# Optimization experiments

Measured on AMD Instinct MI355X. Metric: run time of the kernel, lower is better.

The kernel has to match this reference:

```python
import jax, jax.numpy as jnp
import numpy as np

SCALES = (1, 2, 4, 8, 16)
BETA = 0.25
RESI = 0.5  # Phi(embed_dim, 0.5) -> resi_ratio = 0.5


def _cubic(x):
    # PyTorch bicubic kernel, A = -0.75
    A = -0.75
    x = jnp.abs(x)
    return jnp.where(
        x <= 1.0,
        ((A + 2.0) * x - (A + 3.0)) * x * x + 1.0,
        jnp.where(x < 2.0, A * (((x - 5.0) * x + 8.0) * x - 4.0), 0.0),
    )


def _resize_axis_bicubic(x, axis, out_size):
    # Separable bicubic upsample matching F.interpolate(mode='bicubic', align_corners=False)
    in_size = x.shape[axis]
    scale = in_size / out_size
    src = (jnp.arange(out_size, dtype=jnp.float32) + 0.5) * scale - 0.5
    i0 = jnp.floor(src).astype(jnp.int32)
    frac = src - i0.astype(jnp.float32)
    offs = jnp.arange(-1, 3)
    idx = jnp.clip(i0[:, None] + offs[None, :], 0, in_size - 1)   # [out, 4]
    w = _cubic(frac[:, None] - offs[None, :].astype(jnp.float32))  # [out, 4], rows sum to 1
    g = jnp.take(x, idx, axis=axis)  # axis dim replaced by (out, 4)
    wshape = [1] * g.ndim
    wshape[axis] = out_size
    wshape[axis + 1] = 4
    return jnp.sum(g * w.reshape(wshape), axis=axis + 1)


def _bicubic(x, H, W):
    return _resize_axis_bicubic(_resize_axis_bicubic(x, 2, H), 3, W)


def _phi(x, w, b):
    # Phi: h*(1-r) + conv3x3(h)*r
    y = jax.lax.conv_general_dilated(
        x, w, (1, 1), 'SAME', dimension_numbers=('NCHW', 'OIHW', 'NCHW'))
    return x * (1.0 - RESI) + (y + b[None, :, None, None]) * RESI


def _mse(a, b):
    return jnp.mean((a - b) ** 2)


def _forward(z, emb_weight, phi_w, phi_b):
    B, C, H, W = z.shape
    K = len(SCALES)
    # PhiPartiallyShared ticks for 4 shared convs (K != 4 branch uses 1/3/K spacing)
    ticks = np.linspace(1.0 / (3.0 * 4), 1.0 - 1.0 / (3.0 * 4), 4)
    sg = jax.lax.stop_gradient
    z_d = sg(z)
    z_res = z_d
    z_hat = jnp.zeros_like(z_d)
    emb_sq = jnp.sum(emb_weight * emb_weight, axis=1)  # [n_e]
    loss = jnp.zeros((), z.dtype)
    idx_list = []
    for si, ph in enumerate(SCALES):
        if si != K - 1:
            f = H // ph  # 'area' interpolate == exact average pooling (ph divides H)
            r = z_res.reshape(B, C, ph, f, ph, f).mean(axis=(3, 5))
        else:
            r = z_res
        rf = r.transpose(0, 2, 3, 1).reshape(-1, C)  # [B*ph*ph, C]
        # argmin of cdist == argmin of ||e||^2 - 2 r.e (||r||^2 constant per row)
        d = emb_sq[None, :] - 2.0 * (rf @ emb_weight.T)  # [N, n_e]
        idx = jnp.argmin(d, axis=1)
        q = emb_weight[idx].reshape(B, ph, ph, C).transpose(0, 3, 1, 2)  # [B,C,ph,ph]
        if si != K - 1:
            q = _bicubic(q, H, W)
        pi = int(np.argmin(np.abs(ticks - si / (K - 1))))  # static Phi selection
        q = _phi(q, phi_w[pi], phi_b[pi])
        z_hat = z_hat + q
        z_res = z_res - sg(q)
        idx_list.append(idx.reshape(B, -1))
        loss = loss + BETA * _mse(sg(z_hat), z) + _mse(z_hat, z_d)
    loss = loss / K
    z_hat_st = sg(z_hat - z_d) + z  # straight-through
    return z_hat_st, loss, jnp.concatenate(idx_list, axis=1)


def setup_inputs():
    key = jax.random.key(0)
    k1, k2, k3, k4 = jax.random.split(key, 4)
    z = jax.random.normal(k1, (64, 32, 16, 16), jnp.float32)
    emb_weight = jax.random.normal(k2, (4096, 32), jnp.float32)
    phi_w = jax.random.normal(k3, (4, 32, 32, 3, 3), jnp.float32) * 0.05
    phi_b = jax.random.normal(k4, (4, 32), jnp.float32) * 0.01
    return {"z": z, "emb_weight": emb_weight, "phi_w": phi_w, "phi_b": phi_b}


def reference(z, emb_weight, phi_w, phi_b):
    return _forward(z, emb_weight, phi_w, phi_b)
```

## Files before the change

kernel.cpp:

```cpp
#include <hip/hip_runtime.h>

#define NB 64
#define NC 32
#define NH 16
#define NW 16
#define NE 4096
#define NTOT (NB*NC*NH*NW)
#define IDXW 341
#define GRID 256
#define TPB 1024

typedef float f32x2 __attribute__((ext_vector_type(2)));
typedef float f32x4 __attribute__((ext_vector_type(4)));

__device__ __forceinline__ f32x2 pkfma(f32x2 a, f32x2 b, f32x2 c) {
#if __has_builtin(__builtin_elementwise_fma)
  return __builtin_elementwise_fma(a, b, c);
#else
  return (f32x2){fmaf(a.x, b.x, c.x), fmaf(a.y, b.y, c.y)};
#endif
}

__device__ __forceinline__ double cubicw(double x) {
  const double A = -0.75;
  x = fabs(x);
  if (x <= 1.0) return ((A + 2.0) * x - (A + 3.0)) * x * x + 1.0;
  if (x < 2.0)  return A * (((x - 5.0) * x + 8.0) * x - 4.0);
  return 0.0;
}

__device__ __forceinline__ unsigned monokey(float f) {
  unsigned u = __float_as_uint(f);
  return (u & 0x80000000u) ? ~u : (u | 0x80000000u);
}

__device__ __forceinline__ unsigned aload(unsigned* p) {
  return __hip_atomic_load(p, __ATOMIC_RELAXED, __HIP_MEMORY_SCOPE_AGENT);
}

__device__ __forceinline__ void groupbar(unsigned* fl) {
  __syncthreads();
  if (threadIdx.x == 0) {
    __hip_atomic_fetch_add(fl, 1u, __ATOMIC_RELAXED, __HIP_MEMORY_SCOPE_AGENT);
    while (aload(fl) < 4u) __builtin_amdgcn_s_sleep(1);
  }
  __syncthreads();
}

__global__ __launch_bounds__(TPB)
__attribute__((amdgpu_waves_per_eu(4, 4)))
void k_fused(
    const float* __restrict__ z, const float* __restrict__ emb,
    const float* __restrict__ phi_w, const float* __restrict__ phi_b,
    double* __restrict__ rv64, double* __restrict__ emb_sq,
    double* __restrict__ loss_d, float* __restrict__ emb_ti,
    float* __restrict__ emb_sq32, int* __restrict__ win,
    unsigned* __restrict__ cnt, unsigned* __restrict__ gbar,
    unsigned* __restrict__ flags,
    float* __restrict__ out_zhat, float* __restrict__ out_loss,
    float* __restrict__ out_idx)
{
  __shared__ double lds[8192];
  double* zres = lds;
  char* qreg   = (char*)lds + 16384;
  char* ttreg  = (char*)lds + 49152;

  const int tid = threadIdx.x;
  const int b = blockIdx.x & 63, jq = blockIdx.x >> 6;
  const int co0 = jq * 8;

  if (tid < 16) atomicCAS(&flags[(b << 4) + tid], 0xAAAAAAAAu, 0u);
  if (tid == 0) {
    atomicCAS((unsigned long long*)loss_d, 0xAAAAAAAAAAAAAAAAull, 0ull);
    atomicCAS(cnt, 0xAAAAAAAAu, 0u);
    atomicCAS(gbar, 0xAAAAAAAAu, 0u);
  }

  #pragma unroll
  for (int t = 0; t < 2; t++) {
    int i = t * TPB + tid;
    zres[i] = (double)z[((b * NC + co0) << 8) + i];
  }
  {
    int c0 = blockIdx.x * 16;
    if (tid < 512) {
      int cl = tid >> 5, k = tid & 31;
      emb_ti[(k >> 1) * 8192 + (c0 + cl) * 2 + (k & 1)] = emb[(c0 + cl) * NC + k];
    }
    if (tid < 16) {
      const float* er = emb + (c0 + tid) * NC;
      double s = 0.0;
      #pragma unroll
      for (int j = 0; j < 8; j++)
        s += (double)er[4*j]*er[4*j] + (double)er[4*j+1]*er[4*j+1]
           + (double)er[4*j+2]*er[4*j+2] + (double)er[4*j+3]*er[4*j+3];
      emb_sq[c0 + tid] = s;
      emb_sq32[c0 + tid] = (float)s;
    }
  }
  __syncthreads();
  if (tid == 0) {
    __threadfence();
    __hip_atomic_fetch_add(&flags[(b << 4) + 15], 1u, __ATOMIC_RELAXED,
                           __HIP_MEMORY_SCOPE_AGENT);
    if (jq == 0) {
      while (aload(&flags[(b << 4) + 15]) < 4u) __builtin_amdgcn_s_sleep(1);
      __hip_atomic_fetch_add(gbar, 1u, __ATOMIC_RELAXED,
                             __HIP_MEMORY_SCOPE_AGENT);
      while (aload(gbar) < 64u) __builtin_amdgcn_s_sleep(4);
      __hip_atomic_store(&flags[(b << 4) + 14], 1u, __ATOMIC_RELAXED,
                         __HIP_MEMORY_SCOPE_AGENT);
    } else {
      while (aload(&flags[(b << 4) + 14]) < 1u) __builtin_amdgcn_s_sleep(1);
    }
    __threadfence();
  }
  __syncthreads();

  double bloss = 0.0;
  const int pis[5]  = {0, 1, 2, 2, 3};
  const int offs[5] = {0, 1, 5, 21, 85};

  for (int si = 0; si < 5; si++) {
    const int ph = 1 << si, f = NH / ph, ph2 = ph * ph;
    const int idx_off = offs[si];

    if (si == 4) {
      #pragma unroll
      for (int t = 0; t < 2; t++) {
        int i = t * TPB + tid;
        int pix = i >> 3, cc = i & 7;
        __hip_atomic_store(&rv64[(((b << 8) + pix) << 5) + co0 + cc],
                           zres[cc * 256 + pix],
                           __ATOMIC_RELAXED, __HIP_MEMORY_SCOPE_AGENT);
      }
    } else {
      double* pp = (double*)qreg;
      double* pooled = (double*)(qreg + 8192);
      const int P = (f >= 8) ? 8 : f;
      const int lP = (f >= 8) ? 3 : ((f == 4) ? 2 : 1);
      const int items = 8 * ph2, work = items * P, dpp = f / P;
      if (tid < work) {
        int it = tid >> lP, part = tid & (P - 1);
        int cc = it >> (2 * si), rem = it & (ph2 - 1);
        int y = rem >> si, x = rem & (ph - 1);
        const double* basep = zres + cc * 256 + (y * f) * 16 + x * f;
        double s = 0.0;
        for (int dy = part * dpp; dy < part * dpp + dpp; dy++) {
          const double* rp = basep + dy * 16;
          #pragma unroll 4
          for (int dx = 0; dx < f; dx++) s += rp[dx];
        }
        pp[tid] = s;
      }
      __syncthreads();
      if (tid < items) {
        double s = 0.0;
        for (int p2 = 0; p2 < P; p2++) s += pp[(tid << lP) + p2];
        pooled[tid] = s / (double)(f * f);
      }
      __syncthreads();
      if (tid < items) {
        int rem = tid >> 3, cc = tid & 7;
        __hip_atomic_store(&rv64[(((b << 8) + rem) << 5) + co0 + cc],
                           pooled[cc * ph2 + rem],
                           __ATOMIC_RELAXED, __HIP_MEMORY_SCOPE_AGENT);
      }
    }
    groupbar(&flags[(b << 4) + si * 2]);

    {
      const int count = (ph2 > jq) ? ((ph2 - jq + 3) >> 2) : 0;
      float*  rvt32 = (float*)qreg;
      double* rvt64 = (double*)(qreg + 8192);
      unsigned long long* wdu = (unsigned long long*)(qreg + 24576);
      unsigned short* cand = (unsigned short*)(qreg + 26624);
      for (int t = tid; t < 2048; t += TPB) {
        int m = t >> 5, k = t & 31;
        double v = __hip_atomic_load(&rv64[(((b << 8) + jq + 4 * m) << 5) + k],
                                     __ATOMIC_RELAXED, __HIP_MEMORY_SCOPE_AGENT);
        rvt64[t] = v;
        rvt32[t] = (float)v;
      }
      __syncthreads();
      if (count) {
        const int e0 = tid << 2;
        const f32x4 es4 = *(const f32x4*)(emb_sq32 + e0);
        const int lane = tid & 63, wv_ = tid >> 6;
        for (int m0 = 0; m0 < count; m0 += 8) {
          #pragma unroll
          for (int jg = 0; jg < 2; jg++) {
            f32x4 acc[4];
            #pragma unroll
            for (int j = 0; j < 4; j++) acc[j] = (f32x4){0.f, 0.f, 0.f, 0.f};
            const f32x4* __restrict__ eb = (const f32x4*)emb_ti + (tid << 1);
            #pragma unroll 4
            for (int k2 = 0; k2 < 16; k2++) {
              f32x4 E0 = eb[k2 * 2048];
              f32x4 E1 = eb[k2 * 2048 + 1];
              #pragma unroll
              for (int j = 0; j < 4; j++) {
                f32x2 r2 = *(const f32x2*)(rvt32 + ((m0 + jg * 4 + j) << 5)
                                           + (k2 << 1));
                f32x2 lo = {acc[j].x, acc[j].y}, hi = {acc[j].z, acc[j].w};
                lo = pkfma((f32x2){r2.x, r2.x}, (f32x2){E0.x, E0.z}, lo);
                lo = pkfma((f32x2){r2.y, r2.y}, (f32x2){E0.y, E0.w}, lo);
                hi = pkfma((f32x2){r2.x, r2.x}, (f32x2){E1.x, E1.z}, hi);
                hi = pkfma((f32x2){r2.y, r2.y}, (f32x2){E1.y, E1.w}, hi);
                acc[j] = (f32x4){lo.x, lo.y, hi.x, hi.y};
              }
            }
            #pragma unroll
            for (int j = 0; j < 4; j++) {
              float d0 = es4.x - 2.f * acc[j].x;
              float d1 = es4.y - 2.f * acc[j].y;
              float d2 = es4.z - 2.f * acc[j].z;
              float d3 = es4.w - 2.f * acc[j].w;
              float b1 = d0, b2; int i1 = e0, i2;
              if (d1 < b1) { b2 = b1; i2 = i1; b1 = d1; i1 = e0 + 1; }
              else         { b2 = d1; i2 = e0 + 1; }
              if (d2 < b1) { b2 = b1; i2 = i1; b1 = d2; i1 = e0 + 2; }
              else if (d2 < b2) { b2 = d2; i2 = e0 + 2; }
              if (d3 < b1) { b2 = b1; i2 = i1; b1 = d3; i1 = e0 + 3; }
              else if (d3 < b2) { b2 = d3; i2 = e0 + 3; }
              unsigned long long p1 =
                  ((unsigned long long)monokey(b1) << 32) | (unsigned)i1;
              unsigned long long p2 =
                  ((unsigned long long)monokey(b2) << 32) | (unsigned)i2;
              #pragma unroll
              for (int off = 32; off >= 1; off >>= 1) {
                unsigned long long q1 = __shfl_xor(p1, off, 64);
                unsigned long long q2 = __shfl_xor(p2, off, 64);
                unsigned long long lo = p1 < q1 ? p1 : q1;
                unsigned long long hi = p1 < q1 ? q1 : p1;
                unsigned long long m2 = p2 < q2 ? p2 : q2;
                p1 = lo;
                p2 = hi < m2 ? hi : m2;
              }
              if (lane == 0) {
                int row = (jg << 2) + j;
                wdu[(wv_ << 4) + (row << 1)]     = p1;
                wdu[(wv_ << 4) + (row << 1) + 1] = p2;
              }
            }
          }
          __syncthreads();
          if (tid < 8 && m0 + tid < count) {
            unsigned long long G1 = ~0ull, G2 = ~0ull;
            #pragma unroll
            for (int w = 0; w < 16; w++) {
              unsigned long long a1 = wdu[(w << 4) + (tid << 1)];
              unsigned long long a2 = wdu[(w << 4) + (tid << 1) + 1];
              if (a1 < G1) { G2 = (G1 < a2 ? G1 : a2); G1 = a1; }
              else if (a1 < G2) G2 = a1;
            }
            cand[((m0 + tid) << 1)]     = (unsigned short)(G1 & 0xFFFFu);
            cand[((m0 + tid) << 1) + 1] = (unsigned short)(G2 & 0xFFFFu);
          }
          __syncthreads();
        }
        if (tid < 2 * count) {
          int m = tid >> 1, cs = tid & 1;
          int c = cand[(m << 1) + cs];
          const float* er = emb + (c << 5);
          double dot = 0.0;
          #pragma unroll
          for (int k = 0; k < 32; k++)
            dot = fma(rvt64[(m << 5) + k], (double)er[k], dot);
          double d = emb_sq[c] - 2.0 * dot;
          double doth = __shfl_xor(d, 1, 64);
          int coth = __shfl_xor(c, 1, 64);
          if (cs == 0) {
            int wc = (doth < d || (doth == d && coth < c)) ? coth : c;
            int n = jq + (m << 2);
            __hip_atomic_store(&win[(b << 8) + n], wc,
                               __ATOMIC_RELAXED, __HIP_MEMORY_SCOPE_AGENT);
            out_idx[b * IDXW + idx_off + n] = (float)wc;
          }
        }
      }
    }
    groupbar(&flags[(b << 4) + si * 2 + 1]);

    unsigned short* fidx = (unsigned short*)(ttreg + 12800);
    if (tid < ph2)
      fidx[tid] = (unsigned short)__hip_atomic_load(&win[(b << 8) + tid],
                      __ATOMIC_RELAXED, __HIP_MEMORY_SCOPE_AGENT);
    __syncthreads();

    float* simg = (float*)qreg;
    if (si == 4) {
      for (int i = tid; i < 32 * 256; i += TPB)
        simg[i] = emb[(int)fidx[i & 255] * NC + (i >> 8)];
    } else {
      float* wtab = (float*)(ttreg + 12288);
      int* itab = (int*)(ttreg + 12544);
      double scale = (double)ph / 16.0;
      if (tid < 64) {
        int oy = tid >> 2, kk = tid & 3;
        double src = ((double)oy + 0.5) * scale - 0.5;
        double fi = floor(src);
        if (kk == 0) itab[oy] = (int)fi;
        wtab[tid] = (float)cubicw(src - fi - (double)(kk - 1));
      }
      __syncthreads();
      int CH = (si == 3) ? 16 : 32, nhalf = (si == 3) ? 2 : 1;
      float* qs = (float*)(ttreg + 8192);
      float* tt = (float*)ttreg;
      for (int half = 0; half < nhalf; half++) {
        int c0 = half * CH;
        for (int i = tid; i < CH * ph2; i += TPB) {
          int cc = i >> (2 * si), rem = i & (ph2 - 1);
          qs[i] = emb[(int)fidx[rem] * NC + c0 + cc];
        }
        __syncthreads();
        for (int i = tid; i < CH * 16 * ph; i += TPB) {
          int x = i & (ph - 1), oy = (i >> si) & 15, cc = i >> (4 + si);
          int i0 = itab[oy];
          float s = 0.f;
          #pragma unroll
          for (int k = 0; k < 4; k++) {
            int iy = min(max(i0 + k - 1, 0), ph - 1);
            s = fmaf(wtab[oy * 4 + k], qs[(cc * ph + iy) * ph + x], s);
          }
          tt[i] = s;
        }
        __syncthreads();
        for (int i = tid; i < CH * 256; i += TPB) {
          int ox = i & 15, oy = (i >> 4) & 15, cc = i >> 8;
          int i0 = itab[ox];
          float s = 0.f;
          #pragma unroll
          for (int k = 0; k < 4; k++) {
            int ix = min(max(i0 + k - 1, 0), ph - 1);
            s = fmaf(wtab[ox * 4 + k], tt[(cc * 16 + oy) * ph + ix], s);
          }
          simg[(c0 + cc) * 256 + oy * 16 + ox] = s;
        }
        __syncthreads();
      }
    }
    __syncthreads();

    {
      float* lw2 = (float*)ttreg;
      const float* wsrc = phi_w + (pis[si] * NC + co0) * NC * 9;
      for (int i = tid; i < 2304; i += TPB) {
        int co = i / 288, rem = i - co * 288;
        lw2[(((co >> 1) * 288 + rem) << 1) + (co & 1)] = wsrc[i];
      }
      __syncthreads();
      int pix = tid & 255, sub = tid >> 8;
      int x = pix & 15, y = pix >> 4;
      f32x2 a = {0.f, 0.f};
      const f32x2* wp = (const f32x2*)lw2 + sub * 288;
      for (int ci = 0; ci < NC; ci++) {
        float wv[9];
        #pragma unroll
        for (int ky = 0; ky < 3; ky++) {
          int yy = y + ky - 1;
          #pragma unroll
          for (int kx = 0; kx < 3; kx++) {
            int xx = x + kx - 1;
            wv[ky * 3 + kx] = (yy >= 0 && yy < NH && xx >= 0 && xx < NW)
                              ? simg[(ci << 8) + yy * 16 + xx] : 0.f;
          }
        }
        #pragma unroll
        for (int k = 0; k < 9; k++)
          a = pkfma((f32x2){wv[k], wv[k]}, wp[ci * 9 + k], a);
      }
      double lsum = 0.0;
      #pragma unroll
      for (int jj = 0; jj < 2; jj++) {
        int col = (sub << 1) + jj;
        float aj = jj ? a.y : a.x;
        float val = simg[((co0 + col) << 8) + pix] * 0.5f
                  + (aj + phi_b[pis[si] * NC + co0 + col]) * 0.5f;
        int li = (col << 8) + pix;
        double zr = zres[li] - (double)val;
        zres[li] = zr;
        if (si == 4) {
          int gi = ((b * NC + co0 + col) << 8) + pix;
          out_zhat[gi] = (float)((double)z[gi] - zr);
        }
        lsum += zr * zr;
      }
      __syncthreads();
      #pragma unroll
      for (int off = 32; off >= 1; off >>= 1)
        lsum += __shfl_xor(lsum, off, 64);
      double* red = (double*)qreg;
      if ((tid & 63) == 0) red[tid >> 6] = lsum;
      __syncthreads();
      if (tid < 16) {
        double v = red[tid];
        #pragma unroll
        for (int off = 8; off >= 1; off >>= 1) v += __shfl_xor(v, off, 16);
        if (tid == 0) bloss += v;
      }
      __syncthreads();
    }
  }

  if (tid == 0) {
    double old = unsafeAtomicAdd(loss_d, bloss); (void)old;
    asm volatile("s_waitcnt vmcnt(0)" ::: "memory");
    unsigned n = __hip_atomic_fetch_add(cnt, 1u, __ATOMIC_RELAXED,
                                        __HIP_MEMORY_SCOPE_AGENT);
    if (n == GRID - 1u) {
      double tot = __hip_atomic_load(loss_d, __ATOMIC_RELAXED,
                                     __HIP_MEMORY_SCOPE_AGENT);
      *out_loss = (float)(tot * (1.25 / (5.0 * (double)NTOT)));
    }
  }
}

extern "C" void kernel_launch(void* const* d_in, const int* in_sizes, int n_in,
                              void* d_out, int out_size, void* d_ws, size_t ws_size,
                              hipStream_t stream) {
  const float* z     = (const float*)d_in[0];
  const float* emb   = (const float*)d_in[1];
  const float* phi_w = (const float*)d_in[2];
  const float* phi_b = (const float*)d_in[3];

  float* out      = (float*)d_out;
  float* out_zhat = out;
  float* out_loss = out + NTOT;
  float* out_idx  = out + NTOT + 1;

  double* ws       = (double*)d_ws;
  double* rv64     = ws;
  double* emb_sq   = rv64 + 64 * 256 * NC;
  double* loss_d   = emb_sq + NE;
  float*  emb_ti   = (float*)(loss_d + 2);
  float*  emb_sq32 = emb_ti + NE * NC;
  int*    win      = (int*)(emb_sq32 + NE);
  unsigned* cnt    = (unsigned*)(win + NB * 256);
  unsigned* gbar   = cnt + 1;
  unsigned* flags  = gbar + 1;

  k_fused<<<GRID, TPB, 0, stream>>>(z, emb, phi_w, phi_b,
                                    rv64, emb_sq, loss_d, emb_ti, emb_sq32,
                                    win, cnt, gbar, flags,
                                    out_zhat, out_loss, out_idx);
}
```

Before: 435.6 us.

## Template codebook scan rows, pad conv image in LDS, read conv weights directly

The argmin scan becomes a template on rows per pass. Early scales keep 4 rows, while the last two scales process 16 rows at once, so the 4096-entry codebook is read fewer times. Staging of residual rows now covers only as many as the scale needs. The conv input image is stored in LDS with a zero halo (18x18), which removes bounds checks, and conv weights are read straight from global memory instead of being staged and repacked into LDS. Together these cut codebook traffic and conv overhead, at the cost of more registers, higher LDS use with a reshuffled layout, and uncached weight loads.

```diff
diff --git a/kernel.cpp b/kernel.cpp
--- a/kernel.cpp
+++ b/kernel.cpp
@@ -45,6 +45,108 @@
     while (aload(fl) < 4u) __builtin_amdgcn_s_sleep(1);
   }
   __syncthreads();
+}
+
+
+template<int ROWS>
+__device__ __forceinline__ void scan_phase(
+    int count, int b, int jq, int idx_off, int tid,
+    const float* __restrict__ emb, const float* __restrict__ emb_ti,
+    const float* __restrict__ emb_sq32, const double* __restrict__ emb_sq,
+    float* rvt32, double* rvt64, unsigned long long* wdu,
+    unsigned short* cand, int* __restrict__ win,
+    float* __restrict__ out_idx)
+{
+  if (!count) return;
+  const int e0 = tid << 2;
+  const f32x4 es4 = *(const f32x4*)(emb_sq32 + e0);
+  const int lane = tid & 63, wv_ = tid >> 6;
+  for (int m0 = 0; m0 < count; m0 += ROWS) {
+    f32x4 acc[ROWS];
+    #pragma unroll
+    for (int j = 0; j < ROWS; j++) acc[j] = (f32x4){0.f, 0.f, 0.f, 0.f};
+    const f32x4* __restrict__ eb = (const f32x4*)emb_ti + (tid << 1);
+    #pragma unroll 2
+    for (int k2 = 0; k2 < 16; k2++) {
+      f32x4 E0 = eb[k2 * 2048];
+      f32x4 E1 = eb[k2 * 2048 + 1];
+      #pragma unroll
+      for (int j = 0; j < ROWS; j++) {
+        f32x2 r2 = *(const f32x2*)(rvt32 + ((m0 + j) << 5) + (k2 << 1));
+        f32x2 lo = {acc[j].x, acc[j].y}, hi = {acc[j].z, acc[j].w};
+        lo = pkfma((f32x2){r2.x, r2.x}, (f32x2){E0.x, E0.z}, lo);
+        lo = pkfma((f32x2){r2.y, r2.y}, (f32x2){E0.y, E0.w}, lo);
+        hi = pkfma((f32x2){r2.x, r2.x}, (f32x2){E1.x, E1.z}, hi);
+        hi = pkfma((f32x2){r2.y, r2.y}, (f32x2){E1.y, E1.w}, hi);
+        acc[j] = (f32x4){lo.x, lo.y, hi.x, hi.y};
+      }
+    }
+    #pragma unroll
+    for (int j = 0; j < ROWS; j++) {
+      float d0 = es4.x - 2.f * acc[j].x;
+      float d1 = es4.y - 2.f * acc[j].y;
+      float d2 = es4.z - 2.f * acc[j].z;
+      float d3 = es4.w - 2.f * acc[j].w;
+      float b1 = d0, b2; int i1 = e0, i2;
+      if (d1 < b1) { b2 = b1; i2 = i1; b1 = d1; i1 = e0 + 1; }
+      else         { b2 = d1; i2 = e0 + 1; }
+      if (d2 < b1) { b2 = b1; i2 = i1; b1 = d2; i1 = e0 + 2; }
+      else if (d2 < b2) { b2 = d2; i2 = e0 + 2; }
+      if (d3 < b1) { b2 = b1; i2 = i1; b1 = d3; i1 = e0 + 3; }
+      else if (d3 < b2) { b2 = d3; i2 = e0 + 3; }
+      unsigned long long p1 =
+          ((unsigned long long)monokey(b1) << 32) | (unsigned)i1;
+      unsigned long long p2 =
+          ((unsigned long long)monokey(b2) << 32) | (unsigned)i2;
+      #pragma unroll
+      for (int off = 32; off >= 1; off >>= 1) {
+        unsigned long long q1 = __shfl_xor(p1, off, 64);
+        unsigned long long q2 = __shfl_xor(p2, off, 64);
+        unsigned long long lo = p1 < q1 ? p1 : q1;
+        unsigned long long hi = p1 < q1 ? q1 : p1;
+        unsigned long long m2 = p2 < q2 ? p2 : q2;
+        p1 = lo;
+        p2 = hi < m2 ? hi : m2;
+      }
+      if (lane == 0) {
+        wdu[((wv_ * ROWS + j) << 1)]     = p1;
+        wdu[((wv_ * ROWS + j) << 1) + 1] = p2;
+      }
+    }
+    __syncthreads();
+    if (tid < ROWS && m0 + tid < count) {
+      unsigned long long G1 = ~0ull, G2 = ~0ull;
+      #pragma unroll
+      for (int w = 0; w < 16; w++) {
+        unsigned long long a1 = wdu[((w * ROWS + tid) << 1)];
+        unsigned long long a2 = wdu[((w * ROWS + tid) << 1) + 1];
+        if (a1 < G1) { G2 = (G1 < a2 ? G1 : a2); G1 = a1; }
+        else if (a1 < G2) G2 = a1;
+      }
+      cand[((m0 + tid) << 1)]     = (unsigned short)(G1 & 0xFFFFu);
+      cand[((m0 + tid) << 1) + 1] = (unsigned short)(G2 & 0xFFFFu);
+    }
+    __syncthreads();
+  }
+  if (tid < 2 * count) {
+    int m = tid >> 1, cs = tid & 1;
+    int c = cand[(m << 1) + cs];
+    const float* er = emb + (c << 5);
+    double dot = 0.0;
+    #pragma unroll
+    for (int k = 0; k < 32; k++)
+      dot = fma(rvt64[(m << 5) + k], (double)er[k], dot);
+    double d = emb_sq[c] - 2.0 * dot;
+    double doth = __shfl_xor(d, 1, 64);
+    int coth = __shfl_xor(c, 1, 64);
+    if (cs == 0) {
+      int wc = (doth < d || (doth == d && coth < c)) ? coth : c;
+      int n = jq + (m << 2);
+      __hip_atomic_store(&win[(b << 8) + n], wc,
+                         __ATOMIC_RELAXED, __HIP_MEMORY_SCOPE_AGENT);
+      out_idx[b * IDXW + idx_off + n] = (float)wc;
+    }
+  }
 }
 
 __global__ __launch_bounds__(TPB)
@@ -61,9 +163,8 @@
     float* __restrict__ out_idx)
 {
   __shared__ double lds[8192];
+  char* base = (char*)lds;
   double* zres = lds;
-  char* qreg   = (char*)lds + 16384;
-  char* ttreg  = (char*)lds + 49152;
 
   const int tid = threadIdx.x;
   const int b = blockIdx.x & 63, jq = blockIdx.x >> 6;
@@ -135,8 +236,8 @@
                            __ATOMIC_RELAXED, __HIP_MEMORY_SCOPE_AGENT);
       }
     } else {
-      double* pp = (double*)qreg;
-      double* pooled = (double*)(qreg + 8192);
+      double* pp = (double*)(base + 16384);
+      double* pooled = (double*)(base + 24576);
       const int P = (f >= 8) ? 8 : f;
       const int lP = (f >= 8) ? 3 : ((f == 4) ? 2 : 1);
       const int items = 8 * ph2, work = items * P, dpp = f / P;
@@ -171,11 +272,12 @@
 
     {
       const int count = (ph2 > jq) ? ((ph2 - jq + 3) >> 2) : 0;
-      float*  rvt32 = (float*)qreg;
-      double* rvt64 = (double*)(qreg + 8192);
-      unsigned long long* wdu = (unsigned long long*)(qreg + 24576);
-      unsigned short* cand = (unsigned short*)(qreg + 26624);
-      for (int t = tid; t < 2048; t += TPB) {
+      const int nstage = (count <= 16) ? 16 : 64;
+      float*  rvt32 = (float*)(base + 16384);
+      double* rvt64 = (double*)(base + 24576);
+      unsigned long long* wdu = (unsigned long long*)(base + 40960);
+      unsigned short* cand = (unsigned short*)(base + 45056);
+      for (int t = tid; t < nstage * 32; t += TPB) {
         int m = t >> 5, k = t & 31;
         double v = __hip_atomic_load(&rv64[(((b << 8) + jq + 4 * m) << 5) + k],
                                      __ATOMIC_RELAXED, __HIP_MEMORY_SCOPE_AGENT);
@@ -183,130 +285,45 @@
         rvt32[t] = (float)v;
       }
       __syncthreads();
-      if (count) {
-        const int e0 = tid << 2;
-        const f32x4 es4 = *(const f32x4*)(emb_sq32 + e0);
-        const int lane = tid & 63, wv_ = tid >> 6;
-        for (int m0 = 0; m0 < count; m0 += 8) {
-          #pragma unroll
-          for (int jg = 0; jg < 2; jg++) {
-            f32x4 acc[4];
-            #pragma unroll
-            for (int j = 0; j < 4; j++) acc[j] = (f32x4){0.f, 0.f, 0.f, 0.f};
-            const f32x4* __restrict__ eb = (const f32x4*)emb_ti + (tid << 1);
-            #pragma unroll 4
-            for (int k2 = 0; k2 < 16; k2++) {
-              f32x4 E0 = eb[k2 * 2048];
-              f32x4 E1 = eb[k2 * 2048 + 1];
-              #pragma unroll
-              for (int j = 0; j < 4; j++) {
-                f32x2 r2 = *(const f32x2*)(rvt32 + ((m0 + jg * 4 + j) << 5)
-                                           + (k2 << 1));
-                f32x2 lo = {acc[j].x, acc[j].y}, hi = {acc[j].z, acc[j].w};
-                lo = pkfma((f32x2){r2.x, r2.x}, (f32x2){E0.x, E0.z}, lo);
-                lo = pkfma((f32x2){r2.y, r2.y}, (f32x2){E0.y, E0.w}, lo);
-                hi = pkfma((f32x2){r2.x, r2.x}, (f32x2){E1.x, E1.z}, hi);
-                hi = pkfma((f32x2){r2.y, r2.y}, (f32x2){E1.y, E1.w}, hi);
-                acc[j] = (f32x4){lo.x, lo.y, hi.x, hi.y};
-              }
-            }
-            #pragma unroll
-            for (int j = 0; j < 4; j++) {
-              float d0 = es4.x - 2.f * acc[j].x;
-              float d1 = es4.y - 2.f * acc[j].y;
-              float d2 = es4.z - 2.f * acc[j].z;
-              float d3 = es4.w - 2.f * acc[j].w;
-              float b1 = d0, b2; int i1 = e0, i2;
-              if (d1 < b1) { b2 = b1; i2 = i1; b1 = d1; i1 = e0 + 1; }
-              else         { b2 = d1; i2 = e0 + 1; }
-              if (d2 < b1) { b2 = b1; i2 = i1; b1 = d2; i1 = e0 + 2; }
-              else if (d2 < b2) { b2 = d2; i2 = e0 + 2; }
-              if (d3 < b1) { b2 = b1; i2 = i1; b1 = d3; i1 = e0 + 3; }
-              else if (d3 < b2) { b2 = d3; i2 = e0 + 3; }
-              unsigned long long p1 =
-                  ((unsigned long long)monokey(b1) << 32) | (unsigned)i1;
-              unsigned long long p2 =
-                  ((unsigned long long)monokey(b2) << 32) | (unsigned)i2;
-              #pragma unroll
-              for (int off = 32; off >= 1; off >>= 1) {
-                unsigned long long q1 = __shfl_xor(p1, off, 64);
-                unsigned long long q2 = __shfl_xor(p2, off, 64);
-                unsigned long long lo = p1 < q1 ? p1 : q1;
-                unsigned long long hi = p1 < q1 ? q1 : p1;
-                unsigned long long m2 = p2 < q2 ? p2 : q2;
-                p1 = lo;
-                p2 = hi < m2 ? hi : m2;
-              }
-              if (lane == 0) {
-                int row = (jg << 2) + j;
-                wdu[(wv_ << 4) + (row << 1)]     = p1;
-                wdu[(wv_ << 4) + (row << 1) + 1] = p2;
-              }
-            }
-          }
-          __syncthreads();
-          if (tid < 8 && m0 + tid < count) {
-            unsigned long long G1 = ~0ull, G2 = ~0ull;
-            #pragma unroll
-            for (int w = 0; w < 16; w++) {
-              unsigned long long a1 = wdu[(w << 4) + (tid << 1)];
-              unsigned long long a2 = wdu[(w << 4) + (tid << 1) + 1];
-              if (a1 < G1) { G2 = (G1 < a2 ? G1 : a2); G1 = a1; }
-              else if (a1 < G2) G2 = a1;
-            }
-            cand[((m0 + tid) << 1)]     = (unsigned short)(G1 & 0xFFFFu);
-            cand[((m0 + tid) << 1) + 1] = (unsigned short)(G2 & 0xFFFFu);
-          }
-          __syncthreads();
-        }
-        if (tid < 2 * count) {
-          int m = tid >> 1, cs = tid & 1;
-          int c = cand[(m << 1) + cs];
-          const float* er = emb + (c << 5);
-          double dot = 0.0;
-          #pragma unroll
-          for (int k = 0; k < 32; k++)
-            dot = fma(rvt64[(m << 5) + k], (double)er[k], dot);
-          double d = emb_sq[c] - 2.0 * dot;
-          double doth = __shfl_xor(d, 1, 64);
-          int coth = __shfl_xor(c, 1, 64);
-          if (cs == 0) {
-            int wc = (doth < d || (doth == d && coth < c)) ? coth : c;
-            int n = jq + (m << 2);
-            __hip_atomic_store(&win[(b << 8) + n], wc,
-                               __ATOMIC_RELAXED, __HIP_MEMORY_SCOPE_AGENT);
-            out_idx[b * IDXW + idx_off + n] = (float)wc;
-          }
-        }
-      }
+      if (si < 3)
+        scan_phase<4>(count, b, jq, idx_off, tid, emb, emb_ti, emb_sq32,
+                      emb_sq, rvt32, rvt64, wdu, cand, win, out_idx);
+      else
+        scan_phase<16>(count, b, jq, idx_off, tid, emb, emb_ti, emb_sq32,
+                       emb_sq, rvt32, rvt64, wdu, cand, win, out_idx);
     }
     groupbar(&flags[(b << 4) + si * 2 + 1]);
 
-    unsigned short* fidx = (unsigned short*)(ttreg + 12800);
+    unsigned short* fidx = (unsigned short*)(base + 64320);
     if (tid < ph2)
       fidx[tid] = (unsigned short)__hip_atomic_load(&win[(b << 8) + tid],
                       __ATOMIC_RELAXED, __HIP_MEMORY_SCOPE_AGENT);
     __syncthreads();
 
-    float* simg = (float*)qreg;
+    float* simg = (float*)(base + 16384);
+    for (int i = tid; i < 32 * 324; i += TPB) simg[i] = 0.f;
+    float* wtab = (float*)(base + 64000);
+    int*   itab = (int*)(base + 64256);
+    if (si < 4 && tid < 64) {
+      double scale = (double)ph / 16.0;
+      int oy = tid >> 2, kk = tid & 3;
+      double src = ((double)oy + 0.5) * scale - 0.5;
+      double fi = floor(src);
+      if (kk == 0) itab[oy] = (int)fi;
+      wtab[tid] = (float)cubicw(src - fi - (double)(kk - 1));
+    }
+    __syncthreads();
     if (si == 4) {
-      for (int i = tid; i < 32 * 256; i += TPB)
-        simg[i] = emb[(int)fidx[i & 255] * NC + (i >> 8)];
+      for (int i = tid; i < 32 * 256; i += TPB) {
+        int j = i >> 8, pix = i & 255;
+        simg[j * 324 + (1 + (pix >> 4)) * 18 + 1 + (pix & 15)] =
+            emb[(int)fidx[pix] * NC + j];
+      }
     } else {
-      float* wtab = (float*)(ttreg + 12288);
-      int* itab = (int*)(ttreg + 12544);
-      double scale = (double)ph / 16.0;
-      if (tid < 64) {
-        int oy = tid >> 2, kk = tid & 3;
-        double src = ((double)oy + 0.5) * scale - 0.5;
-        double fi = floor(src);
-        if (kk == 0) itab[oy] = (int)fi;
-        wtab[tid] = (float)cubicw(src - fi - (double)(kk - 1));
-      }
-      __syncthreads();
-      int CH = (si == 3) ? 16 : 32, nhalf = (si == 3) ? 2 : 1;
-      float* qs = (float*)(ttreg + 8192);
-      float* tt = (float*)ttreg;
+      const int CH = (si <= 1) ? 32 : ((si == 2) ? 16 : 8);
+      const int nhalf = 32 / CH;
+      float* tt = (float*)(base + 57856);
+      float* qs = (float*)(base + 61952);
       for (int half = 0; half < nhalf; half++) {
         int c0 = half * CH;
         for (int i = tid; i < CH * ph2; i += TPB) {
@@ -335,7 +352,7 @@
             int ix = min(max(i0 + k - 1, 0), ph - 1);
             s = fmaf(wtab[ox * 4 + k], tt[(cc * 16 + oy) * ph + ix], s);
           }
-          simg[(c0 + cc) * 256 + oy * 16 + ox] = s;
+          simg[(c0 + cc) * 324 + (1 + oy) * 18 + 1 + ox] = s;
         }
         __syncthreads();
       }
@@ -343,39 +360,30 @@
     __syncthreads();
 
     {
-      float* lw2 = (float*)ttreg;
-      const float* wsrc = phi_w + (pis[si] * NC + co0) * NC * 9;
-      for (int i = tid; i < 2304; i += TPB) {
-        int co = i / 288, rem = i - co * 288;
-        lw2[(((co >> 1) * 288 + rem) << 1) + (co & 1)] = wsrc[i];
-      }
-      __syncthreads();
       int pix = tid & 255, sub = tid >> 8;
       int x = pix & 15, y = pix >> 4;
-      f32x2 a = {0.f, 0.f};
-      const f32x2* wp = (const f32x2*)lw2 + sub * 288;
+      float a0 = 0.f, a1 = 0.f;
+      const float* wp0 = phi_w + ((pis[si] * NC + co0 + sub * 2) * NC) * 9;
+      const float* wp1 = wp0 + NC * 9;
       for (int ci = 0; ci < NC; ci++) {
+        const float* sb = simg + ci * 324 + y * 18 + x;
         float wv[9];
         #pragma unroll
-        for (int ky = 0; ky < 3; ky++) {
-          int yy = y + ky - 1;
+        for (int ky = 0; ky < 3; ky++)
           #pragma unroll
-          for (int kx = 0; kx < 3; kx++) {
-            int xx = x + kx - 1;
-            wv[ky * 3 + kx] = (yy >= 0 && yy < NH && xx >= 0 && xx < NW)
-                              ? simg[(ci << 8) + yy * 16 + xx] : 0.f;
-          }
-        }
+          for (int kx = 0; kx < 3; kx++)
+            wv[ky * 3 + kx] = sb[ky * 18 + kx];
         #pragma unroll
-        for (int k = 0; k < 9; k++)
-          a = pkfma((f32x2){wv[k], wv[k]}, wp[ci * 9 + k], a);
+        for (int k = 0; k < 9; k++) a0 = fmaf(wv[k], wp0[ci * 9 + k], a0);
+        #pragma unroll
+        for (int k = 0; k < 9; k++) a1 = fmaf(wv[k], wp1[ci * 9 + k], a1);
       }
       double lsum = 0.0;
       #pragma unroll
       for (int jj = 0; jj < 2; jj++) {
         int col = (sub << 1) + jj;
-        float aj = jj ? a.y : a.x;
-        float val = simg[((co0 + col) << 8) + pix] * 0.5f
+        float aj = jj ? a1 : a0;
+        float val = simg[(co0 + col) * 324 + (1 + y) * 18 + 1 + x] * 0.5f
                   + (aj + phi_b[pis[si] * NC + co0 + col]) * 0.5f;
         int li = (col << 8) + pix;
         double zr = zres[li] - (double)val;
@@ -390,7 +398,7 @@
       #pragma unroll
       for (int off = 32; off >= 1; off >>= 1)
         lsum += __shfl_xor(lsum, off, 64);
-      double* red = (double*)qreg;
+      double* red = (double*)(base + 64832);
       if ((tid & 63) == 0) red[tid >> 6] = lsum;
       __syncthreads();
       if (tid < 16) {
```

Result: slower. 1.693 ms (+288.7%).
